# Optimization experiments

Hardware: AMD Instinct MI355X
Metric: run time of the kernel (lower is better)

Reference implementation:

```python
import jax, jax.numpy as jnp
import numpy as np

B, N, CIN, CD, NE = 64, 256, 768, 32, 8192

def setup_inputs() -> dict:
    key = jax.random.key(0)
    ks = jax.random.split(key, 8)
    z = jax.random.normal(ks[0], (B, N, CIN), dtype=jnp.float32)
    # Embedding weight: trunc_normal_(mean=0, std=1, a=-3, b=3)
    emb_weight = jax.random.truncated_normal(ks[1], -3.0, 3.0, (NE, CD)).astype(jnp.float32)
    # Linears stored as [in, out] so y = x @ W + b
    W_compress = jax.random.normal(ks[2], (CIN, CD), dtype=jnp.float32) / np.sqrt(CIN)
    b_compress = jnp.zeros((CD,), dtype=jnp.float32)
    W_ct = jax.random.normal(ks[3], (CD, CD), dtype=jnp.float32) / np.sqrt(CD)
    b_ct = jnp.zeros((CD,), dtype=jnp.float32)
    W_expand = jax.random.normal(ks[4], (CD, CIN), dtype=jnp.float32) / np.sqrt(CD)
    b_expand = jnp.zeros((CIN,), dtype=jnp.float32)
    return {"z": z, "emb_weight": emb_weight, "W_compress": W_compress,
            "b_compress": b_compress, "W_ct": W_ct, "b_ct": b_ct,
            "W_expand": W_expand, "b_expand": b_expand}

def reference(z, emb_weight, W_compress, b_compress, W_ct, b_ct, W_expand, b_expand):
    sg = jax.lax.stop_gradient
    # torch uses embedding.weight.data -> detached codebook input
    implicit_codebook = sg(emb_weight) @ W_ct + b_ct              # [NE, CD]
    zc = z @ W_compress + b_compress                              # [B, N, CD]
    z_flat = zc.reshape(-1, zc.shape[-1])                         # [B*N, CD]
    # squared distance: ||z||^2 + ||c||^2 - 2 z.c
    d = (jnp.sum(z_flat ** 2, axis=1, keepdims=True)
         + jnp.sum(implicit_codebook ** 2, axis=1)
         - 2.0 * jnp.einsum('bd,nd->bn', z_flat, implicit_codebook))  # [B*N, NE]
    indices = jnp.argmin(d, axis=1)                               # [B*N]
    z_q = implicit_codebook[indices]                              # [B*N, CD]
    # training-path losses (codebook + 2.0 * commitment)
    loss = (jnp.mean((sg(z_q) - z_flat) ** 2)
            + 2.0 * jnp.mean((z_q - sg(z_flat)) ** 2))
    # straight-through estimator
    z_st = sg(z_q) + z_flat - sg(z_flat)
    out = z_st.reshape(zc.shape) @ W_expand + b_expand            # [B, N, CIN]
    return out, loss
```

## Files before the change

kernel.cpp:

```cpp
#include <hip/hip_runtime.h>

constexpr int CIN = 768;
constexpr int CD  = 32;
constexpr int NE  = 8192;
constexpr int M   = 16384;
constexpr int SCH = 64;
constexpr int CPC = NE / SCH;
constexpr int PTB = 128;
#define MARGIN 0.05f

typedef short short8 __attribute__((ext_vector_type(8)));
typedef float f32x4  __attribute__((ext_vector_type(4)));

__device__ inline void split_bf16(float x, unsigned short& h, unsigned short& l) {
  unsigned u = __float_as_uint(x);
  unsigned hb = (u + 0x7FFFu + ((u >> 16) & 1u)) >> 16;
  float hf = __uint_as_float(hb << 16);
  float r = x - hf;
  unsigned u2 = __float_as_uint(r);
  unsigned lb = (u2 + 0x7FFFu + ((u2 >> 16) & 1u)) >> 16;
  h = (unsigned short)hb;
  l = (unsigned short)lb;
}

__device__ inline void gload_lds16(const void* g, void* l) {
  __builtin_amdgcn_global_load_lds(
      (const __attribute__((address_space(1))) unsigned int*)g,
      (__attribute__((address_space(3))) unsigned int*)l, 16, 0, 0);
}

__global__ __launch_bounds__(256, 2) void k_pre(
    const float* __restrict__ emb, const float* __restrict__ Wct,
    const float* __restrict__ bct,
    const float* __restrict__ z, const float* __restrict__ Wc,
    const float* __restrict__ bc, const float* __restrict__ We,
    float* __restrict__ cb, float* __restrict__ cnorm,
    unsigned short* __restrict__ ch, unsigned short* __restrict__ cl,
    float* __restrict__ zc, unsigned short* __restrict__ zh,
    unsigned short* __restrict__ zl,
    unsigned short* __restrict__ WeTh, unsigned short* __restrict__ WeTl) {
  __shared__ float smem[6912];
  const int t = threadIdx.x;
  if (blockIdx.x >= 1536) {
    const int n = (blockIdx.x - 1536) * 256 + t;
    #pragma unroll
    for (int k = 0; k < CD; ++k) {
      unsigned short h, l;
      split_bf16(We[(long)k * CIN + n], h, l);
      WeTh[n * CD + k] = h;
      WeTl[n * CD + k] = l;
    }
    return;
  }
  if (blockIdx.x >= 512) {
    for (int i = t; i < CD * CD; i += 256) smem[i] = Wct[i];
    __syncthreads();
    const int g   = (blockIdx.x - 512) * 256 + t;
    const int row = g >> 5;
    const int col = g & 31;
    float acc = bct[col];
    const float* er = emb + row * CD;
    #pragma unroll
    for (int k = 0; k < CD; ++k) acc = fmaf(er[k], smem[k * CD + col], acc);
    cb[g] = acc;
    unsigned short h, l;
    split_bf16(acc, h, l);
    ch[g] = h; cl[g] = l;
    float v = acc * acc;
    #pragma unroll
    for (int m = 16; m >= 1; m >>= 1) v += __shfl_xor(v, m, 64);
    if (col == 0) cnorm[row] = v;
    return;
  }
  const int p   = t & 15;
  const int spl = t >> 4;
  const int wid = t >> 6;
  const int r0  = blockIdx.x * 32;
  const int row = r0 + 2 * p;
  const float* z0 = z + (long)row * CIN + spl * 48;
  const float* z1 = z0 + CIN;
  float acc0[32], acc1[32];
  if (spl == 0) {
    #pragma unroll
    for (int c = 0; c < 32; ++c) { acc0[c] = bc[c]; acc1[c] = bc[c]; }
  } else {
    #pragma unroll
    for (int c = 0; c < 32; ++c) { acc0[c] = 0.f; acc1[c] = 0.f; }
  }
  for (int cch = 0; cch < 4; ++cch) {
    float4 a0[3], a1[3];
    #pragma unroll
    for (int q = 0; q < 3; ++q) {
      a0[q] = *(const float4*)(z0 + cch * 12 + q * 4);
      a1[q] = *(const float4*)(z1 + cch * 12 + q * 4);
    }
    #pragma unroll
    for (int i = 0; i < 6; ++i) {
      const int f   = t + i * 256;
      const int sp2 = f / 96;
      const int rem = f - sp2 * 96;
      const int kk  = rem >> 3;
      const int c4  = rem & 7;
      const float4 wvv = *(const float4*)(Wc + ((sp2 * 48 + cch * 12 + kk) << 5) + (c4 << 2));
      *(float4*)(smem + sp2 * 432 + kk * 36 + (c4 << 2)) = wvv;
    }
    __syncthreads();
    const float* wsb = smem + spl * 432;
    #pragma unroll
    for (int q = 0; q < 3; ++q) {
      #pragma unroll
      for (int j = 0; j < 4; ++j) {
        const float zk0 = (j == 0) ? a0[q].x : (j == 1) ? a0[q].y : (j == 2) ? a0[q].z : a0[q].w;
        const float zk1 = (j == 0) ? a1[q].x : (j == 1) ? a1[q].y : (j == 2) ? a1[q].z : a1[q].w;
        const float* wr = wsb + (q * 4 + j) * 36;
        #pragma unroll
        for (int c4i = 0; c4i < 8; ++c4i) {
          const float4 wvv = *(const float4*)(wr + (c4i << 2));
          acc0[c4i * 4 + 0] = fmaf(zk0, wvv.x, acc0[c4i * 4 + 0]);
          acc0[c4i * 4 + 1] = fmaf(zk0, wvv.y, acc0[c4i * 4 + 1]);
          acc0[c4i * 4 + 2] = fmaf(zk0, wvv.z, acc0[c4i * 4 + 2]);
          acc0[c4i * 4 + 3] = fmaf(zk0, wvv.w, acc0[c4i * 4 + 3]);
          acc1[c4i * 4 + 0] = fmaf(zk1, wvv.x, acc1[c4i * 4 + 0]);
          acc1[c4i * 4 + 1] = fmaf(zk1, wvv.y, acc1[c4i * 4 + 1]);
          acc1[c4i * 4 + 2] = fmaf(zk1, wvv.z, acc1[c4i * 4 + 2]);
          acc1[c4i * 4 + 3] = fmaf(zk1, wvv.w, acc1[c4i * 4 + 3]);
        }
      }
    }
    __syncthreads();
  }
  #pragma unroll
  for (int mk = 16; mk <= 32; mk <<= 1) {
    #pragma unroll
    for (int c = 0; c < 32; ++c) {
      acc0[c] += __shfl_xor(acc0[c], mk, 64);
      acc1[c] += __shfl_xor(acc1[c], mk, 64);
    }
  }
  if (((t >> 4) & 3) == 0) {
    float* rr0 = smem + wid * 1152 + (2 * p) * 36;
    float* rr1 = rr0 + 36;
    #pragma unroll
    for (int c4i = 0; c4i < 8; ++c4i) {
      float4 v0, v1;
      v0.x = acc0[c4i * 4 + 0]; v0.y = acc0[c4i * 4 + 1];
      v0.z = acc0[c4i * 4 + 2]; v0.w = acc0[c4i * 4 + 3];
      v1.x = acc1[c4i * 4 + 0]; v1.y = acc1[c4i * 4 + 1];
      v1.z = acc1[c4i * 4 + 2]; v1.w = acc1[c4i * 4 + 3];
      *(float4*)(rr0 + (c4i << 2)) = v0;
      *(float4*)(rr1 + (c4i << 2)) = v1;
    }
  }
  __syncthreads();
  const int grow = t >> 3;
  const int gc4  = t & 7;
  const float* rb = smem + grow * 36 + (gc4 << 2);
  const float4 s0 = *(const float4*)(rb);
  const float4 s1 = *(const float4*)(rb + 1152);
  const float4 s2 = *(const float4*)(rb + 2304);
  const float4 s3 = *(const float4*)(rb + 3456);
  float4 sv;
  sv.x = ((s0.x + s1.x) + s2.x) + s3.x;
  sv.y = ((s0.y + s1.y) + s2.y) + s3.y;
  sv.z = ((s0.z + s1.z) + s2.z) + s3.z;
  sv.w = ((s0.w + s1.w) + s2.w) + s3.w;
  const long idx = (long)(r0 + grow) * CD + (gc4 << 2);
  *(float4*)(zc + idx) = sv;
  ushort4 h4, l4;
  split_bf16(-2.f * sv.x, h4.x, l4.x);
  split_bf16(-2.f * sv.y, h4.y, l4.y);
  split_bf16(-2.f * sv.z, h4.z, l4.z);
  split_bf16(-2.f * sv.w, h4.w, l4.w);
  *(ushort4*)(zh + idx) = h4;
  *(ushort4*)(zl + idx) = l4;
}

__global__ __launch_bounds__(256) void k_argmin(
    const unsigned short* __restrict__ zh, const unsigned short* __restrict__ zl,
    const unsigned short* __restrict__ ch, const unsigned short* __restrict__ cl,
    const float* __restrict__ cnorm,
    float* __restrict__ pd) {
  __shared__ __align__(16) unsigned short chs[CPC * CD];
  __shared__ __align__(16) unsigned short cls[CPC * CD];
  const int pb   = blockIdx.x & (M / PTB - 1);
  const int cid  = blockIdx.x >> 7;
  const int lane = threadIdx.x & 63;
  const int wv   = threadIdx.x >> 6;
  const int col  = lane & 15;
  const int quad = lane >> 4;
  const int p0   = pb * PTB + wv * 32;

  const char* chg = (const char*)ch + (long)cid * (CPC * CD * 2);
  const char* clg = (const char*)cl + (long)cid * (CPC * CD * 2);
  #pragma unroll
  for (int s = 0; s < 2; ++s) {
    const int lo = s * 4096 + wv * 1024;
    gload_lds16(chg + lo + lane * 16, (char*)chs + lo);
    gload_lds16(clg + lo + lane * 16, (char*)cls + lo);
  }

  const short8 Ah0 = *(const short8*)(zh + (long)(p0 + col) * CD + quad * 8);
  const short8 Al0 = *(const short8*)(zl + (long)(p0 + col) * CD + quad * 8);
  const short8 Ah1 = *(const short8*)(zh + (long)(p0 + 16 + col) * CD + quad * 8);
  const short8 Al1 = *(const short8*)(zl + (long)(p0 + 16 + col) * CD + quad * 8);

  const int jb = cid * CPC;
  float cnv[8];
  #pragma unroll
  for (int tt = 0; tt < 8; ++tt) cnv[tt] = cnorm[jb + tt * 16 + col];

  float bd0[4], bd1[4];
  #pragma unroll
  for (int r = 0; r < 4; ++r) { bd0[r] = 1e30f; bd1[r] = 1e30f; }

  __syncthreads();

  #pragma unroll
  for (int tt = 0; tt < 8; ++tt) {
    const short8 Bh = *(const short8*)(chs + (tt * 16 + col) * CD + quad * 8);
    const short8 Bl = *(const short8*)(cls + (tt * 16 + col) * CD + quad * 8);
    const f32x4 c4 = {cnv[tt], cnv[tt], cnv[tt], cnv[tt]};
    f32x4 g0 = __builtin_amdgcn_mfma_f32_16x16x32_bf16(Ah0, Bh, c4, 0, 0, 0);
    g0 = __builtin_amdgcn_mfma_f32_16x16x32_bf16(Ah0, Bl, g0, 0, 0, 0);
    g0 = __builtin_amdgcn_mfma_f32_16x16x32_bf16(Al0, Bh, g0, 0, 0, 0);
    f32x4 g1 = __builtin_amdgcn_mfma_f32_16x16x32_bf16(Ah1, Bh, c4, 0, 0, 0);
    g1 = __builtin_amdgcn_mfma_f32_16x16x32_bf16(Ah1, Bl, g1, 0, 0, 0);
    g1 = __builtin_amdgcn_mfma_f32_16x16x32_bf16(Al1, Bh, g1, 0, 0, 0);
    #pragma unroll
    for (int r = 0; r < 4; ++r) {
      bd0[r] = fminf(bd0[r], g0[r]);
      bd1[r] = fminf(bd1[r], g1[r]);
    }
  }

  #pragma unroll
  for (int mm = 1; mm <= 8; mm <<= 1) {
    #pragma unroll
    for (int r = 0; r < 4; ++r) {
      bd0[r] = fminf(bd0[r], __shfl_xor(bd0[r], mm, 64));
      bd1[r] = fminf(bd1[r], __shfl_xor(bd1[r], mm, 64));
    }
  }
  if (col == 0) {
    #pragma unroll
    for (int r = 0; r < 4; ++r) {
      const int pA = p0 + quad * 4 + r;
      pd[(long)pA * SCH + cid] = bd0[r];
      const int pB = pA + 16;
      pd[(long)pB * SCH + cid] = bd1[r];
    }
  }
}

__global__ __launch_bounds__(256) void k_rescue(
    const float* __restrict__ zc, const float* __restrict__ cb,
    const float* __restrict__ cnorm,
    const float* __restrict__ pd,
    float* __restrict__ zq, unsigned short* __restrict__ zqh,
    unsigned short* __restrict__ zql, float* __restrict__ lpart) {
  const int lane = threadIdx.x & 63;
  const int wv   = threadIdx.x >> 6;
  const int p    = blockIdx.x * 4 + wv;

  const float m = pd[(long)p * SCH + lane];
  float dstar = m;
  #pragma unroll
  for (int mm = 1; mm <= 32; mm <<= 1) dstar = fminf(dstar, __shfl_xor(dstar, mm, 64));
  unsigned long long mask = __ballot(m <= dstar + MARGIN);

  float zr[CD];
  {
    const float4* z4 = (const float4*)(zc + (long)p * CD);
    #pragma unroll
    for (int q = 0; q < 8; ++q) {
      float4 v = z4[q];
      zr[4 * q + 0] = v.x; zr[4 * q + 1] = v.y; zr[4 * q + 2] = v.z; zr[4 * q + 3] = v.w;
    }
  }

  float bd = 1e30f;
  int   bj = 0x7fffffff;
  while (mask) {
    const int c = (int)__builtin_ctzll(mask);
    mask &= mask - 1;
    #pragma unroll
    for (int u = 0; u < 2; ++u) {
      const int j = c * CPC + u * 64 + lane;
      const float4* crow = (const float4*)(cb + (long)j * CD);
      float acc = 0.f;
      #pragma unroll
      for (int q = 0; q < 8; ++q) {
        float4 cv = crow[q];
        acc = fmaf(zr[4 * q + 0], cv.x, acc);
        acc = fmaf(zr[4 * q + 1], cv.y, acc);
        acc = fmaf(zr[4 * q + 2], cv.z, acc);
        acc = fmaf(zr[4 * q + 3], cv.w, acc);
      }
      const float d = fmaf(-2.f, acc, cnorm[j]);
      if (d < bd) { bd = d; bj = j; }
    }
  }
  #pragma unroll
  for (int mm = 1; mm <= 32; mm <<= 1) {
    const float od = __shfl_xor(bd, mm, 64);
    const int   oj = __shfl_xor(bj, mm, 64);
    if (od < bd || (od == bd && oj < bj)) { bd = od; bj = oj; }
  }

  float ls = 0.f;
  if (lane < 32) {
    const float cv = cb[(long)bj * CD + lane];
    const float zv = zc[(long)p * CD + lane];
    zq[(long)p * CD + lane] = cv;
    unsigned short hh, ll;
    split_bf16(cv, hh, ll);
    zqh[(long)p * CD + lane] = hh;
    zql[(long)p * CD + lane] = ll;
    const float df = cv - zv;
    ls = df * df;
  }
  #pragma unroll
  for (int mm = 1; mm <= 32; mm <<= 1) ls += __shfl_xor(ls, mm, 64);
  if (lane == 0) lpart[p] = ls;
}

__global__ __launch_bounds__(256) void k_expand(
    const unsigned short* __restrict__ zqh, const unsigned short* __restrict__ zql,
    const unsigned short* __restrict__ WeTh, const unsigned short* __restrict__ WeTl,
    const float* __restrict__ be,
    const float* __restrict__ lpart,
    float* __restrict__ out,
    float* __restrict__ out_loss) {
  __shared__ double redd[4];
  const int t = threadIdx.x;
  if (blockIdx.x == 1024) {
    double v = 0.0;
    for (int k = t; k < M; k += 256) v += (double)lpart[k];
    #pragma unroll
    for (int mm = 1; mm <= 32; mm <<= 1) v += __shfl_xor(v, mm, 64);
    if ((t & 63) == 0) redd[t >> 6] = v;
    __syncthreads();
    if (t == 0)
      out_loss[0] = (float)(3.0 * (redd[0] + redd[1] + redd[2] + redd[3]) / (double)(M * CD));
    return;
  }
  const int lane = t & 63;
  const int wv   = t >> 6;
  const int col  = lane & 15;
  const int quad = lane >> 4;
  const int r0   = blockIdx.x * 16;

  const short8 Ah = *(const short8*)(zqh + (long)(r0 + col) * CD + quad * 8);
  const short8 Al = *(const short8*)(zql + (long)(r0 + col) * CD + quad * 8);

  #pragma unroll
  for (int tt = 0; tt < 12; ++tt) {
    const int n0 = (wv * 12 + tt) * 16;
    const short8 Bh = *(const short8*)(WeTh + (long)(n0 + col) * CD + quad * 8);
    const short8 Bl = *(const short8*)(WeTl + (long)(n0 + col) * CD + quad * 8);
    const float bv = be[n0 + col];
    const f32x4 c4 = {bv, bv, bv, bv};
    f32x4 g = __builtin_amdgcn_mfma_f32_16x16x32_bf16(Ah, Bh, c4, 0, 0, 0);
    g = __builtin_amdgcn_mfma_f32_16x16x32_bf16(Ah, Bl, g, 0, 0, 0);
    g = __builtin_amdgcn_mfma_f32_16x16x32_bf16(Al, Bh, g, 0, 0, 0);
    #pragma unroll
    for (int r = 0; r < 4; ++r)
      out[(long)(r0 + quad * 4 + r) * CIN + n0 + col] = g[r];
  }
}

extern "C" void kernel_launch(void* const* d_in, const int* in_sizes, int n_in,
                              void* d_out, int out_size, void* d_ws, size_t ws_size,
                              hipStream_t stream) {
  const float* z   = (const float*)d_in[0];
  const float* emb = (const float*)d_in[1];
  const float* Wc  = (const float*)d_in[2];
  const float* bc  = (const float*)d_in[3];
  const float* Wct = (const float*)d_in[4];
  const float* bct = (const float*)d_in[5];
  const float* We  = (const float*)d_in[6];
  const float* be  = (const float*)d_in[7];
  float* out = (float*)d_out;

  float* cb    = (float*)d_ws;
  float* cnorm = cb + NE * CD;
  float* zc    = cnorm + NE;
  float* zq    = zc + M * CD;
  float* pd    = zq + M * CD;
  float* lpart = pd + (long)M * SCH;
  unsigned short* zh   = (unsigned short*)(lpart + M);
  unsigned short* zl   = zh + M * CD;
  unsigned short* ch   = zl + M * CD;
  unsigned short* cl   = ch + NE * CD;
  unsigned short* zqh  = cl + NE * CD;
  unsigned short* zql  = zqh + M * CD;
  unsigned short* WeTh = zql + M * CD;
  unsigned short* WeTl = WeTh + CIN * CD;

  k_pre<<<1539, 256, 0, stream>>>(emb, Wct, bct, z, Wc, bc, We,
                                  cb, cnorm, ch, cl, zc, zh, zl, WeTh, WeTl);
  k_argmin<<<(M / PTB) * SCH, 256, 0, stream>>>(zh, zl, ch, cl, cnorm, pd);
  k_rescue<<<M / 4, 256, 0, stream>>>(zc, cb, cnorm, pd, zq, zqh, zql, lpart);
  k_expand<<<1024 + 1, 256, 0, stream>>>(zqh, zql, WeTh, WeTl, be, lpart,
                                         out, out + (long)M * CIN);
}
```

Baseline: 221.1 us.

## Move compress GEMM to split-bf16 MFMA kernel with pretransposed weights

Replaces the FP32 FMA-based z@W_compress in the fused pre-kernel with a separate k_compress kernel that splits z and a pre-transposed, pre-split W_compress into bf16 hi/lo parts and uses 16x16x32 bf16 MFMA (three products per tile), with a cross-wave LDS reduction. The codebook, We-transpose and new Wc-transpose work move into a lighter k_light kernel. This aims to cut the ALU cost of the compress GEMM, which reads 50MB of z. The cost is an extra kernel launch, a serial Wc transpose done by one block, and a possible small precision loss from dropping the lo*lo term.

```diff
diff --git a/kernel.cpp b/kernel.cpp
--- a/kernel.cpp
+++ b/kernel.cpp
@@ -29,33 +29,20 @@
       (__attribute__((address_space(3))) unsigned int*)l, 16, 0, 0);
 }
 
-__global__ __launch_bounds__(256, 2) void k_pre(
+__global__ __launch_bounds__(256) void k_light(
     const float* __restrict__ emb, const float* __restrict__ Wct,
-    const float* __restrict__ bct,
-    const float* __restrict__ z, const float* __restrict__ Wc,
-    const float* __restrict__ bc, const float* __restrict__ We,
+    const float* __restrict__ bct, const float* __restrict__ Wc,
+    const float* __restrict__ We,
     float* __restrict__ cb, float* __restrict__ cnorm,
     unsigned short* __restrict__ ch, unsigned short* __restrict__ cl,
-    float* __restrict__ zc, unsigned short* __restrict__ zh,
-    unsigned short* __restrict__ zl,
-    unsigned short* __restrict__ WeTh, unsigned short* __restrict__ WeTl) {
-  __shared__ float smem[6912];
+    unsigned short* __restrict__ WeTh, unsigned short* __restrict__ WeTl,
+    unsigned short* __restrict__ WcTh, unsigned short* __restrict__ WcTl) {
+  __shared__ float smem[CD * CD];
   const int t = threadIdx.x;
-  if (blockIdx.x >= 1536) {
-    const int n = (blockIdx.x - 1536) * 256 + t;
-    #pragma unroll
-    for (int k = 0; k < CD; ++k) {
-      unsigned short h, l;
-      split_bf16(We[(long)k * CIN + n], h, l);
-      WeTh[n * CD + k] = h;
-      WeTl[n * CD + k] = l;
-    }
-    return;
-  }
-  if (blockIdx.x >= 512) {
+  if (blockIdx.x < 1024) {
     for (int i = t; i < CD * CD; i += 256) smem[i] = Wct[i];
     __syncthreads();
-    const int g   = (blockIdx.x - 512) * 256 + t;
+    const int g   = blockIdx.x * 256 + t;
     const int row = g >> 5;
     const int col = g & 31;
     float acc = bct[col];
@@ -72,107 +59,114 @@
     if (col == 0) cnorm[row] = v;
     return;
   }
-  const int p   = t & 15;
-  const int spl = t >> 4;
-  const int wid = t >> 6;
-  const int r0  = blockIdx.x * 32;
-  const int row = r0 + 2 * p;
-  const float* z0 = z + (long)row * CIN + spl * 48;
-  const float* z1 = z0 + CIN;
-  float acc0[32], acc1[32];
-  if (spl == 0) {
-    #pragma unroll
-    for (int c = 0; c < 32; ++c) { acc0[c] = bc[c]; acc1[c] = bc[c]; }
+  if (blockIdx.x < 1027) {
+    const int n = (blockIdx.x - 1024) * 256 + t;
+    #pragma unroll
+    for (int k = 0; k < CD; ++k) {
+      unsigned short h, l;
+      split_bf16(We[(long)k * CIN + n], h, l);
+      WeTh[n * CD + k] = h;
+      WeTl[n * CD + k] = l;
+    }
+    return;
+  }
+  {
+    const int n  = t >> 3;
+    const int k0 = (t & 7) * 96;
+    for (int k = k0; k < k0 + 96; ++k) {
+      unsigned short h, l;
+      split_bf16(Wc[k * CD + n], h, l);
+      WcTh[n * CIN + k] = h;
+      WcTl[n * CIN + k] = l;
+    }
+  }
+}
+
+__global__ __launch_bounds__(256) void k_compress(
+    const float* __restrict__ z,
+    const unsigned short* __restrict__ WcTh, const unsigned short* __restrict__ WcTl,
+    const float* __restrict__ bc,
+    float* __restrict__ zc, unsigned short* __restrict__ zh,
+    unsigned short* __restrict__ zl) {
+  __shared__ float ps[3 * 544];
+  const int t    = threadIdx.x;
+  const int lane = t & 63;
+  const int wv   = t >> 6;
+  const int n    = lane & 15;
+  const int quad = lane >> 4;
+  const int r0   = blockIdx.x * 16;
+
+  const float* za = z + (long)(r0 + n) * CIN + wv * 192 + quad * 8;
+  const unsigned short* bh0 = WcTh + n * CIN + wv * 192 + quad * 8;
+  const unsigned short* bl0 = WcTl + n * CIN + wv * 192 + quad * 8;
+  const unsigned short* bh1 = bh0 + 16 * CIN;
+  const unsigned short* bl1 = bl0 + 16 * CIN;
+
+  f32x4 acc0, acc1;
+  if (wv == 0) {
+    const float b0 = bc[n];
+    const float b1 = bc[n + 16];
+    acc0 = (f32x4){b0, b0, b0, b0};
+    acc1 = (f32x4){b1, b1, b1, b1};
   } else {
-    #pragma unroll
-    for (int c = 0; c < 32; ++c) { acc0[c] = 0.f; acc1[c] = 0.f; }
-  }
-  for (int cch = 0; cch < 4; ++cch) {
-    float4 a0[3], a1[3];
-    #pragma unroll
-    for (int q = 0; q < 3; ++q) {
-      a0[q] = *(const float4*)(z0 + cch * 12 + q * 4);
-      a1[q] = *(const float4*)(z1 + cch * 12 + q * 4);
-    }
-    #pragma unroll
-    for (int i = 0; i < 6; ++i) {
-      const int f   = t + i * 256;
-      const int sp2 = f / 96;
-      const int rem = f - sp2 * 96;
-      const int kk  = rem >> 3;
-      const int c4  = rem & 7;
-      const float4 wvv = *(const float4*)(Wc + ((sp2 * 48 + cch * 12 + kk) << 5) + (c4 << 2));
-      *(float4*)(smem + sp2 * 432 + kk * 36 + (c4 << 2)) = wvv;
-    }
-    __syncthreads();
-    const float* wsb = smem + spl * 432;
-    #pragma unroll
-    for (int q = 0; q < 3; ++q) {
-      #pragma unroll
-      for (int j = 0; j < 4; ++j) {
-        const float zk0 = (j == 0) ? a0[q].x : (j == 1) ? a0[q].y : (j == 2) ? a0[q].z : a0[q].w;
-        const float zk1 = (j == 0) ? a1[q].x : (j == 1) ? a1[q].y : (j == 2) ? a1[q].z : a1[q].w;
-        const float* wr = wsb + (q * 4 + j) * 36;
-        #pragma unroll
-        for (int c4i = 0; c4i < 8; ++c4i) {
-          const float4 wvv = *(const float4*)(wr + (c4i << 2));
-          acc0[c4i * 4 + 0] = fmaf(zk0, wvv.x, acc0[c4i * 4 + 0]);
-          acc0[c4i * 4 + 1] = fmaf(zk0, wvv.y, acc0[c4i * 4 + 1]);
-          acc0[c4i * 4 + 2] = fmaf(zk0, wvv.z, acc0[c4i * 4 + 2]);
-          acc0[c4i * 4 + 3] = fmaf(zk0, wvv.w, acc0[c4i * 4 + 3]);
-          acc1[c4i * 4 + 0] = fmaf(zk1, wvv.x, acc1[c4i * 4 + 0]);
-          acc1[c4i * 4 + 1] = fmaf(zk1, wvv.y, acc1[c4i * 4 + 1]);
-          acc1[c4i * 4 + 2] = fmaf(zk1, wvv.z, acc1[c4i * 4 + 2]);
-          acc1[c4i * 4 + 3] = fmaf(zk1, wvv.w, acc1[c4i * 4 + 3]);
-        }
-      }
-    }
-    __syncthreads();
-  }
-  #pragma unroll
-  for (int mk = 16; mk <= 32; mk <<= 1) {
-    #pragma unroll
-    for (int c = 0; c < 32; ++c) {
-      acc0[c] += __shfl_xor(acc0[c], mk, 64);
-      acc1[c] += __shfl_xor(acc1[c], mk, 64);
-    }
-  }
-  if (((t >> 4) & 3) == 0) {
-    float* rr0 = smem + wid * 1152 + (2 * p) * 36;
-    float* rr1 = rr0 + 36;
-    #pragma unroll
-    for (int c4i = 0; c4i < 8; ++c4i) {
-      float4 v0, v1;
-      v0.x = acc0[c4i * 4 + 0]; v0.y = acc0[c4i * 4 + 1];
-      v0.z = acc0[c4i * 4 + 2]; v0.w = acc0[c4i * 4 + 3];
-      v1.x = acc1[c4i * 4 + 0]; v1.y = acc1[c4i * 4 + 1];
-      v1.z = acc1[c4i * 4 + 2]; v1.w = acc1[c4i * 4 + 3];
-      *(float4*)(rr0 + (c4i << 2)) = v0;
-      *(float4*)(rr1 + (c4i << 2)) = v1;
+    acc0 = (f32x4){0.f, 0.f, 0.f, 0.f};
+    acc1 = (f32x4){0.f, 0.f, 0.f, 0.f};
+  }
+
+  #pragma unroll
+  for (int kt = 0; kt < 6; ++kt) {
+    const float4 za0 = *(const float4*)(za + kt * 32);
+    const float4 za1 = *(const float4*)(za + kt * 32 + 4);
+    short8 Ah, Al;
+    {
+      unsigned short h, l;
+      split_bf16(za0.x, h, l); Ah[0] = (short)h; Al[0] = (short)l;
+      split_bf16(za0.y, h, l); Ah[1] = (short)h; Al[1] = (short)l;
+      split_bf16(za0.z, h, l); Ah[2] = (short)h; Al[2] = (short)l;
+      split_bf16(za0.w, h, l); Ah[3] = (short)h; Al[3] = (short)l;
+      split_bf16(za1.x, h, l); Ah[4] = (short)h; Al[4] = (short)l;
+      split_bf16(za1.y, h, l); Ah[5] = (short)h; Al[5] = (short)l;
+      split_bf16(za1.z, h, l); Ah[6] = (short)h; Al[6] = (short)l;
+      split_bf16(za1.w, h, l); Ah[7] = (short)h; Al[7] = (short)l;
+    }
+    const short8 Bh0 = *(const short8*)(bh0 + kt * 32);
+    const short8 Bl0 = *(const short8*)(bl0 + kt * 32);
+    const short8 Bh1 = *(const short8*)(bh1 + kt * 32);
+    const short8 Bl1 = *(const short8*)(bl1 + kt * 32);
+    acc0 = __builtin_amdgcn_mfma_f32_16x16x32_bf16(Ah, Bh0, acc0, 0, 0, 0);
+    acc0 = __builtin_amdgcn_mfma_f32_16x16x32_bf16(Ah, Bl0, acc0, 0, 0, 0);
+    acc0 = __builtin_amdgcn_mfma_f32_16x16x32_bf16(Al, Bh0, acc0, 0, 0, 0);
+    acc1 = __builtin_amdgcn_mfma_f32_16x16x32_bf16(Ah, Bh1, acc1, 0, 0, 0);
+    acc1 = __builtin_amdgcn_mfma_f32_16x16x32_bf16(Ah, Bl1, acc1, 0, 0, 0);
+    acc1 = __builtin_amdgcn_mfma_f32_16x16x32_bf16(Al, Bh1, acc1, 0, 0, 0);
+  }
+
+  if (wv != 0) {
+    float* pp = ps + (wv - 1) * 544;
+    #pragma unroll
+    for (int r = 0; r < 4; ++r) {
+      const int row = quad * 4 + r;
+      pp[row * 17 + n]       = acc0[r];
+      pp[272 + row * 17 + n] = acc1[r];
     }
   }
   __syncthreads();
-  const int grow = t >> 3;
-  const int gc4  = t & 7;
-  const float* rb = smem + grow * 36 + (gc4 << 2);
-  const float4 s0 = *(const float4*)(rb);
-  const float4 s1 = *(const float4*)(rb + 1152);
-  const float4 s2 = *(const float4*)(rb + 2304);
-  const float4 s3 = *(const float4*)(rb + 3456);
-  float4 sv;
-  sv.x = ((s0.x + s1.x) + s2.x) + s3.x;
-  sv.y = ((s0.y + s1.y) + s2.y) + s3.y;
-  sv.z = ((s0.z + s1.z) + s2.z) + s3.z;
-  sv.w = ((s0.w + s1.w) + s2.w) + s3.w;
-  const long idx = (long)(r0 + grow) * CD + (gc4 << 2);
-  *(float4*)(zc + idx) = sv;
-  ushort4 h4, l4;
-  split_bf16(-2.f * sv.x, h4.x, l4.x);
-  split_bf16(-2.f * sv.y, h4.y, l4.y);
-  split_bf16(-2.f * sv.z, h4.z, l4.z);
-  split_bf16(-2.f * sv.w, h4.w, l4.w);
-  *(ushort4*)(zh + idx) = h4;
-  *(ushort4*)(zl + idx) = l4;
+  if (wv == 0) {
+    #pragma unroll
+    for (int r = 0; r < 4; ++r) {
+      const int row = quad * 4 + r;
+      const float v0 = ((acc0[r] + ps[row * 17 + n]) + ps[544 + row * 17 + n])
+                       + ps[1088 + row * 17 + n];
+      const float v1 = ((acc1[r] + ps[272 + row * 17 + n]) + ps[816 + row * 17 + n])
+                       + ps[1360 + row * 17 + n];
+      const long i0 = (long)(r0 + row) * CD + n;
+      zc[i0]      = v0;
+      zc[i0 + 16] = v1;
+      unsigned short h, l;
+      split_bf16(-2.f * v0, h, l); zh[i0] = h;      zl[i0] = l;
+      split_bf16(-2.f * v1, h, l); zh[i0 + 16] = h; zl[i0 + 16] = l;
+    }
+  }
 }
 
 __global__ __launch_bounds__(256) void k_argmin(
@@ -396,9 +390,12 @@
   unsigned short* zql  = zqh + M * CD;
   unsigned short* WeTh = zql + M * CD;
   unsigned short* WeTl = WeTh + CIN * CD;
-
-  k_pre<<<1539, 256, 0, stream>>>(emb, Wct, bct, z, Wc, bc, We,
-                                  cb, cnorm, ch, cl, zc, zh, zl, WeTh, WeTl);
+  unsigned short* WcTh = WeTl + CIN * CD;
+  unsigned short* WcTl = WcTh + CIN * CD;
+
+  k_light<<<1028, 256, 0, stream>>>(emb, Wct, bct, Wc, We,
+                                    cb, cnorm, ch, cl, WeTh, WeTl, WcTh, WcTl);
+  k_compress<<<M / 16, 256, 0, stream>>>(z, WcTh, WcTl, bc, zc, zh, zl);
   k_argmin<<<(M / PTB) * SCH, 256, 0, stream>>>(zh, zl, ch, cl, cnorm, pd);
   k_rescue<<<M / 4, 256, 0, stream>>>(zc, cb, cnorm, pd, zq, zqh, zql, lpart);
   k_expand<<<1024 + 1, 256, 0, stream>>>(zqh, zql, WeTh, WeTl, be, lpart,
```

After: 233.0 us. 5.4% more time.
